# Kernel tuning notes

Hardware: AMD Instinct MI355X
Metric: run time of the kernel (lower is better)

Reference implementation:

```python
import jax, jax.numpy as jnp
import numpy as np

K = 7          # kernel_size
D = 1          # dilation
P = (D * (K - 1) + 1) // 2  # reflect padding = 3
N = 2
C_IN = 256
REL = 16
OUT = 256
SHARE = 8
H = 56
W = 56


def _unfold(x, k=K, d=D, p=P):
    # x: [n, c, h, w] -> [n, c, k*k, h*w], reflection-padded local windows
    n, c, h, w = x.shape
    xp = jnp.pad(x, ((0, 0), (0, 0), (p, p), (p, p)), mode='reflect')
    cols = [xp[:, :, i * d:i * d + h, j * d:j * d + w]
            for i in range(k) for j in range(k)]
    return jnp.stack(cols, axis=2).reshape(n, c, k * k, h * w)


def _conv1x1(x, w, b=None):
    # 1x1 conv == channel contraction; x: [n, c, *spatial]
    y = jnp.einsum('oc,nc...->no...', w, x)
    if b is not None:
        y = y + b.reshape((1, -1) + (1,) * (y.ndim - 2))
    return y


def _bn(x, g, b, eps=1e-5):
    # training-mode batchnorm over (N, *spatial) per channel; x: [n, c, a, b]
    m = x.mean(axis=(0, 2, 3), keepdims=True)
    v = x.var(axis=(0, 2, 3), keepdims=True)
    xh = (x - m) * jax.lax.rsqrt(v + eps)
    return xh * g.reshape(1, -1, 1, 1) + b.reshape(1, -1, 1, 1)


def _position(h, w):
    lw = jnp.broadcast_to(jnp.linspace(-1.0, 1.0, w)[None, :], (h, w))
    lh = jnp.broadcast_to(jnp.linspace(-1.0, 1.0, h)[:, None], (h, w))
    return jnp.stack([lw, lh], 0)[None]  # [1, 2, h, w]


def setup_inputs() -> dict:
    key = jax.random.key(0)
    ks = jax.random.split(key, 16)
    def rn(k, shape, s=0.05):
        return jax.random.normal(k, shape, jnp.float32) * s
    return dict(
        x=jax.random.normal(ks[0], (N, C_IN, H, W), jnp.float32),
        w1=rn(ks[1], (REL, C_IN)), b1=rn(ks[2], (REL,)),
        w2=rn(ks[3], (REL, C_IN)), b2=rn(ks[4], (REL,)),
        w3=rn(ks[5], (OUT, C_IN)), b3=rn(ks[6], (OUT,)),
        wp=rn(ks[7], (2, 2)), bp=rn(ks[8], (2,)),
        g1=jnp.ones(REL + 2, jnp.float32), be1=jnp.zeros(REL + 2, jnp.float32),
        cw1=rn(ks[9], (REL, REL + 2)),
        g2=jnp.ones(REL, jnp.float32), be2=jnp.zeros(REL, jnp.float32),
        cw2=rn(ks[10], (OUT // SHARE, REL)), cb2=rn(ks[11], (OUT // SHARE,)),
    )


def reference(x, w1, b1, w2, b2, w3, b3, wp, bp,
              g1, be1, cw1, g2, be2, cw2, cb2):
    n, _, h, w = x.shape
    hw = h * w
    x1 = _conv1x1(x, w1, b1)   # [n, rel, h, w]
    x2 = _conv1x1(x, w2, b2)   # [n, rel, h, w]
    x3 = _conv1x1(x, w3, b3)   # [n, out, h, w]
    pos = _conv1x1(_position(h, w), wp, bp)  # [1, 2, h, w]
    # Subtraction2: center query minus unfolded keys -> [n, rel, k^2, hw]
    sub2 = x1.reshape(n, REL, 1, hw) - _unfold(x2)
    # Subtraction on position: center minus neighbors -> [1, 2, k^2, hw]
    subp = pos.reshape(1, 2, 1, hw) - _unfold(pos)
    subp = jnp.broadcast_to(subp, (n, 2, K * K, hw))
    t = jnp.concatenate([sub2, subp], axis=1)           # [n, rel+2, k^2, hw]
    t = jax.nn.relu(_bn(t, g1, be1))
    t = _conv1x1(t, cw1)                                # [n, rel, k^2, hw]
    t = jax.nn.relu(_bn(t, g2, be2))
    wlog = _conv1x1(t, cw2, cb2)                        # [n, out//share, k^2, hw]
    ww = jax.nn.softmax(wlog, axis=-2)                  # softmax over k^2
    # Aggregation: gather values over windows and weight per share-group
    u3 = _unfold(x3).reshape(n, OUT // SHARE, SHARE, K * K, hw)
    out = jnp.einsum('ngskq,ngkq->ngsq', u3, ww).reshape(n, OUT, h, w)
    return out
```

## Files before the change

kernel.cpp:

```cpp
#include <hip/hip_runtime.h>
#include <hip/hip_bf16.h>
#include <cstdint>

#define HWS 3136
#define WID 56
#define NKQ 307328.0f
#define X3SCALE 2048.0f
#define X3INV   (1.0f / 2048.0f)
#define WQ      65535.0f

#define S_CW1 0
#define S_CW2 288
#define S_CB2 800
#define S_WP  832
#define S_G1  836
#define S_BE1 854
#define S_G2  872
#define S_BE2 888
#define S_TOT 904
#define NWT   73728

__device__ __forceinline__ int refl(int i) {
  if (i < 0) i = -i;
  if (i >= WID) i = 2 * WID - 2 - i;
  return i;
}

__global__ __launch_bounds__(256) void k_prep(
    const float* __restrict__ w1, const float* __restrict__ w2,
    const float* __restrict__ w3,
    const float* __restrict__ cw1, const float* __restrict__ cw2,
    const float* __restrict__ cb2, const float* __restrict__ wp,
    const float* __restrict__ g1, const float* __restrict__ be1,
    const float* __restrict__ g2, const float* __restrict__ be2,
    float* __restrict__ small, float* __restrict__ wT)
{
  int e = blockIdx.x * 256 + threadIdx.x;
  if (e < S_TOT) {
    float v;
    if (e < S_CW2)      v = cw1[e];
    else if (e < S_CB2) v = cw2[e - S_CW2];
    else if (e < S_WP)  v = cb2[e - S_CB2];
    else if (e < S_G1)  v = wp [e - S_WP];
    else if (e < S_BE1) v = g1 [e - S_G1];
    else if (e < S_G2)  v = be1[e - S_BE1];
    else if (e < S_BE2) v = g2 [e - S_G2];
    else                v = be2[e - S_BE2];
    small[e] = v;
  }
  int et = e - S_TOT;
  if (et >= 0 && et < NWT) {
    int c = et / 288, r = et - (et / 288) * 288;
    float v = (r < 16) ? w1[r * 256 + c]
            : (r < 32) ? w2[(r - 16) * 256 + c]
                       : w3[(r - 32) * 256 + c];
    wT[et] = v;
  }
}

__global__ __launch_bounds__(64) void k_proj(
    const float* __restrict__ x, const float* __restrict__ wT,
    const float* __restrict__ b1, const float* __restrict__ b2,
    const float* __restrict__ b3,
    float* __restrict__ x1t, float* __restrict__ x2t, short* __restrict__ x3i)
{
  const int lane = threadIdx.x;
  const int r0  = (blockIdx.x & 15) * 18;
  const int pck = blockIdx.x >> 4;
  const int P = pck * 64 + lane;
  const int n = P / HWS;

  float acc[18];
  #pragma unroll
  for (int i = 0; i < 18; i++) {
    int r = r0 + i;
    acc[i] = (r < 16) ? b1[r] : (r < 32) ? b2[r - 16] : b3[r - 32];
  }

  const float* xc = x + (size_t)n * 256 * HWS + (P - n * HWS);
  const float* wt0 = wT + r0;
  #pragma unroll 8
  for (int c = 0; c < 256; c++) {
    float xv = xc[(size_t)c * HWS];
    const float* wt = wt0 + c * 288;
    #pragma unroll
    for (int i = 0; i < 18; i++)
      acc[i] = fmaf(wt[i], xv, acc[i]);
  }

  #pragma unroll
  for (int i = 0; i < 18; i++) {
    int r = r0 + i;
    if (r < 16)
      x1t[(size_t)P * 16 + r] = acc[i];
    else if (r < 32)
      x2t[(size_t)P * 16 + (r - 16)] = acc[i];
    else {
      float cl = fminf(fmaxf(acc[i], -15.9f), 15.9f);
      x3i[(size_t)P * 256 + (r - 32)] = (short)__float2int_rn(cl * X3SCALE);
    }
  }
}

__global__ __launch_bounds__(256) void k_stats1(
    const float* __restrict__ x1t, const float* __restrict__ x2t,
    const float* __restrict__ small, float* __restrict__ gsum1)
{
  __shared__ float red[4][36];
  const int tid = threadIdx.x;
  const int bid = blockIdx.x;
  const int n = bid / 196;
  const int r = bid % 196;
  const int k = r >> 2, quar = r & 3;
  const int ki = k / 7 - 3, kj = k % 7 - 3;
  const float wp00 = small[S_WP+0], wp01 = small[S_WP+1];
  const float wp10 = small[S_WP+2], wp11 = small[S_WP+3];
  float s[18], ss[18];
  #pragma unroll
  for (int i = 0; i < 18; i++) { s[i] = 0.f; ss[i] = 0.f; }

  for (int qq = tid; qq < 784; qq += 256) {
    int q = quar * 784 + qq;
    int y = q / WID, xx = q - y * WID;
    int ny = refl(y + ki), nx = refl(xx + kj);
    int nb = ny * WID + nx;
    const float4* a = (const float4*)(x1t + (size_t)(n * HWS + q) * 16);
    const float4* b = (const float4*)(x2t + (size_t)(n * HWS + nb) * 16);
    #pragma unroll
    for (int r4 = 0; r4 < 4; r4++) {
      float4 av = a[r4], bv = b[r4];
      float v;
      v = av.x - bv.x; s[r4*4+0] += v; ss[r4*4+0] += v * v;
      v = av.y - bv.y; s[r4*4+1] += v; ss[r4*4+1] += v * v;
      v = av.z - bv.z; s[r4*4+2] += v; ss[r4*4+2] += v * v;
      v = av.w - bv.w; s[r4*4+3] += v; ss[r4*4+3] += v * v;
    }
    float dlw = (float)(xx - nx) * (2.f / 55.f);
    float dlh = (float)(y - ny) * (2.f / 55.f);
    float v16 = wp00 * dlw + wp01 * dlh;
    float v17 = wp10 * dlw + wp11 * dlh;
    s[16] += v16; ss[16] += v16 * v16;
    s[17] += v17; ss[17] += v17 * v17;
  }

  #pragma unroll
  for (int i = 0; i < 18; i++) {
    #pragma unroll
    for (int off = 32; off > 0; off >>= 1) {
      s[i]  += __shfl_down(s[i], off);
      ss[i] += __shfl_down(ss[i], off);
    }
  }
  const int wvv = tid >> 6, lane = tid & 63;
  if (lane == 0) {
    #pragma unroll
    for (int i = 0; i < 18; i++) { red[wvv][i] = s[i]; red[wvv][18 + i] = ss[i]; }
  }
  __syncthreads();
  if (tid < 36) {
    float t = red[0][tid] + red[1][tid] + red[2][tid] + red[3][tid];
    atomicAdd(&gsum1[tid], t);
  }
}

__global__ __launch_bounds__(256) void k_stats2(
    const float* __restrict__ x1t, const float* __restrict__ x2t,
    const float* __restrict__ small,
    const float* __restrict__ gsum1, float* __restrict__ gsum2)
{
  __shared__ float red[4][32];
  const int tid = threadIdx.x;
  const float inv = 1.f / NKQ;
  float sc1r[18], sh1r[18];
  #pragma unroll
  for (int c = 0; c < 18; c++) {
    float m = gsum1[c] * inv;
    float var = gsum1[18 + c] * inv - m * m;
    float sc = small[S_G1 + c] * rsqrtf(var + 1e-5f);
    sc1r[c] = sc; sh1r[c] = small[S_BE1 + c] - m * sc;
  }

  const int bid = blockIdx.x;
  const int n = bid / 196;
  const int r = bid % 196;
  const int k = r >> 2, quar = r & 3;
  const int ki = k / 7 - 3, kj = k % 7 - 3;
  const float wp00 = small[S_WP+0], wp01 = small[S_WP+1];
  const float wp10 = small[S_WP+2], wp11 = small[S_WP+3];
  const float* cw1f = small + S_CW1;
  float s[16], ss[16];
  #pragma unroll
  for (int i = 0; i < 16; i++) { s[i] = 0.f; ss[i] = 0.f; }

  for (int qq = tid; qq < 784; qq += 256) {
    int q = quar * 784 + qq;
    int y = q / WID, xx = q - y * WID;
    int ny = refl(y + ki), nx = refl(xx + kj);
    int nb = ny * WID + nx;
    float t1v[18];
    const float4* a4 = (const float4*)(x1t + (size_t)(n * HWS + q) * 16);
    const float4* b4 = (const float4*)(x2t + (size_t)(n * HWS + nb) * 16);
    #pragma unroll
    for (int r4 = 0; r4 < 4; r4++) {
      float4 av = a4[r4], bv = b4[r4];
      t1v[r4*4+0] = av.x - bv.x; t1v[r4*4+1] = av.y - bv.y;
      t1v[r4*4+2] = av.z - bv.z; t1v[r4*4+3] = av.w - bv.w;
    }
    float dlw = (float)(xx - nx) * (2.f / 55.f);
    float dlh = (float)(y - ny) * (2.f / 55.f);
    t1v[16] = wp00 * dlw + wp01 * dlh;
    t1v[17] = wp10 * dlw + wp11 * dlh;
    #pragma unroll
    for (int c = 0; c < 18; c++) t1v[c] = fmaxf(fmaf(t1v[c], sc1r[c], sh1r[c]), 0.f);
    #pragma unroll
    for (int r2 = 0; r2 < 16; r2++) {
      float acc = 0.f;
      #pragma unroll
      for (int c = 0; c < 18; c++) acc = fmaf(cw1f[r2 * 18 + c], t1v[c], acc);
      s[r2] += acc; ss[r2] += acc * acc;
    }
  }

  #pragma unroll
  for (int i = 0; i < 16; i++) {
    #pragma unroll
    for (int off = 32; off > 0; off >>= 1) {
      s[i]  += __shfl_down(s[i], off);
      ss[i] += __shfl_down(ss[i], off);
    }
  }
  const int wvv = tid >> 6, lane = tid & 63;
  if (lane == 0) {
    #pragma unroll
    for (int i = 0; i < 16; i++) { red[wvv][i] = s[i]; red[wvv][16 + i] = ss[i]; }
  }
  __syncthreads();
  if (tid < 32) {
    float t = red[0][tid] + red[1][tid] + red[2][tid] + red[3][tid];
    atomicAdd(&gsum2[tid], t);
  }
}

__global__ __launch_bounds__(256) void k_final(
    const float* __restrict__ x1t, const float* __restrict__ x2t,
    const short* __restrict__ x3i, const float* __restrict__ small,
    const float* __restrict__ gsum1, const float* __restrict__ gsum2,
    float* __restrict__ outf)
{
  __shared__ unsigned short wws[4][49][34];
  __shared__ int nbs[4][49];
  __shared__ float sc1s[18], sh1s[18], sc2s[16], sh2s[16];

  const int tid = threadIdx.x;
  const int lane = tid & 63;
  const int wv = tid >> 6;
  const float inv = 1.f / NKQ;

  if (tid < 18) {
    float m = gsum1[tid] * inv;
    float var = gsum1[18 + tid] * inv - m * m;
    float sc = small[S_G1 + tid] * rsqrtf(var + 1e-5f);
    sc1s[tid] = sc; sh1s[tid] = small[S_BE1 + tid] - m * sc;
  } else if (tid >= 32 && tid < 48) {
    int c = tid - 32;
    float m = gsum2[c] * inv;
    float var = gsum2[16 + c] * inv - m * m;
    float sc = small[S_G2 + c] * rsqrtf(var + 1e-5f);
    sc2s[c] = sc; sh2s[c] = small[S_BE2 + c] - m * sc;
  }
  __syncthreads();

  const int P = blockIdx.x * 4 + wv;
  const int n = P / HWS, q = P % HWS;
  const int y = q / WID, xx = q - y * WID;

  const bool valid = lane < 49;
  const int kk = valid ? lane : 48;
  const int ki = kk / 7 - 3, kj = kk % 7 - 3;
  const int ny = refl(y + ki), nx = refl(xx + kj);
  const int nb = ny * WID + nx;
  if (valid) nbs[wv][lane] = nb;

  float t1v[18];
  {
    const float4* a4 = (const float4*)(x1t + (size_t)(n * HWS + q) * 16);
    const float4* b4 = (const float4*)(x2t + (size_t)(n * HWS + nb) * 16);
    #pragma unroll
    for (int r4 = 0; r4 < 4; r4++) {
      float4 av = a4[r4], bv = b4[r4];
      t1v[r4*4+0] = av.x - bv.x; t1v[r4*4+1] = av.y - bv.y;
      t1v[r4*4+2] = av.z - bv.z; t1v[r4*4+3] = av.w - bv.w;
    }
    float dlw = (float)(xx - nx) * (2.f / 55.f);
    float dlh = (float)(y - ny) * (2.f / 55.f);
    t1v[16] = small[S_WP+0] * dlw + small[S_WP+1] * dlh;
    t1v[17] = small[S_WP+2] * dlw + small[S_WP+3] * dlh;
  }
  #pragma unroll
  for (int c = 0; c < 18; c++)
    t1v[c] = fmaxf(fmaf(t1v[c], sc1s[c], sh1s[c]), 0.f);

  float t2v[16];
  #pragma unroll
  for (int r = 0; r < 16; r++) {
    float acc = 0.f;
    #pragma unroll
    for (int c = 0; c < 18; c++) acc = fmaf(small[S_CW1 + r * 18 + c], t1v[c], acc);
    t2v[r] = fmaxf(fmaf(acc, sc2s[r], sh2s[r]), 0.f);
  }

  #pragma unroll
  for (int g = 0; g < 32; g++) {
    float acc = small[S_CB2 + g];
    #pragma unroll
    for (int r = 0; r < 16; r++) acc = fmaf(small[S_CW2 + g * 16 + r], t2v[r], acc);
    float e = valid ? __expf(acc) : 0.f;
    float s = e;
    #pragma unroll
    for (int off = 32; off >= 1; off >>= 1) s += __shfl_xor(s, off);
    if (valid)
      wws[wv][lane][g] = (unsigned short)__float2uint_rn(e / s * WQ);
  }
  __syncthreads();

  const short* x3p = x3i + (size_t)n * HWS * 256;
  const int* nbp = nbs[wv];
  const unsigned short (*wq)[34] = wws[wv];
  const int g0 = lane >> 3;
  float acc4[4] = {0.f, 0.f, 0.f, 0.f};
  #pragma unroll 7
  for (int k = 0; k < 49; k++) {
    const short* row = x3p + (size_t)nbp[k] * 256;
    #pragma unroll
    for (int ch = 0; ch < 4; ch++) {
      float w = (float)wq[k][ch * 8 + g0];
      acc4[ch] = fmaf(w, (float)row[ch * 64 + lane], acc4[ch]);
    }
  }
  const float osc = X3INV / WQ;
  #pragma unroll
  for (int ch = 0; ch < 4; ch++) {
    int o = ch * 64 + lane;
    outf[(size_t)(n * 256 + o) * HWS + q] = acc4[ch] * osc;
  }
}

extern "C" void kernel_launch(void* const* d_in, const int* in_sizes, int n_in,
                              void* d_out, int out_size, void* d_ws, size_t ws_size,
                              hipStream_t stream) {
  (void)in_sizes; (void)n_in; (void)out_size; (void)ws_size;
  char* ws = (char*)d_ws;
  float* gsum1 = (float*)(ws + 0);
  float* gsum2 = (float*)(ws + 160);
  float* small = (float*)(ws + 512);
  float* x1t   = (float*)(ws + 4608);
  float* x2t   = (float*)(ws + 406016);
  short* x3i   = (short*)(ws + 807424);
  float* outf  = (float*)d_out;
  float* wT    = (float*)d_out;

  const float* x   = (const float*)d_in[0];
  const float* w1  = (const float*)d_in[1];
  const float* b1  = (const float*)d_in[2];
  const float* w2  = (const float*)d_in[3];
  const float* b2  = (const float*)d_in[4];
  const float* w3  = (const float*)d_in[5];
  const float* b3  = (const float*)d_in[6];
  const float* wp  = (const float*)d_in[7];
  const float* g1  = (const float*)d_in[9];
  const float* be1 = (const float*)d_in[10];
  const float* cw1 = (const float*)d_in[11];
  const float* g2  = (const float*)d_in[12];
  const float* be2 = (const float*)d_in[13];
  const float* cw2 = (const float*)d_in[14];
  const float* cb2 = (const float*)d_in[15];

  hipMemsetAsync(d_ws, 0, 512, stream);
  k_prep<<<292, 256, 0, stream>>>(w1, w2, w3, cw1, cw2, cb2, wp,
                                  g1, be1, g2, be2, small, wT);
  k_proj<<<1568, 64, 0, stream>>>(x, wT, b1, b2, b3, x1t, x2t, x3i);
  k_stats1<<<392, 256, 0, stream>>>(x1t, x2t, small, gsum1);
  k_stats2<<<392, 256, 0, stream>>>(x1t, x2t, small, gsum1, gsum2);
  k_final<<<1568, 256, 0, stream>>>(x1t, x2t, x3i, small, gsum1, gsum2, outf);
}
```

Measured before the change: 200.9 us.

## Compute BN1 stats via box-filter algebra, defer softmax normalization, vectorize aggregation

Replaces the 49-offset brute-force pass for the first batchnorm statistics with an algebraic expansion. Sums of (x1 - x2_nb) and its square are rebuilt from x1 sums, x1 times a 7x7 reflect box sum of x2 (separable row and column passes), and x2 weighted by reflect multiplicity counts. The final kernel stores unnormalized exp weights in fp16 and divides by their accumulated sum at the end, which removes the per-group wave shuffle reduction. Each lane now loads four contiguous channels through an int2 read. stats2 gets twice as many blocks, and scratch space in the output buffer holds the box sums. The costs are extra launches and the fp32 cancellation risk in the 49*sum minus cross-term formula.

```diff
diff --git a/kernel.cpp b/kernel.cpp
--- a/kernel.cpp
+++ b/kernel.cpp
@@ -1,5 +1,6 @@
 #include <hip/hip_runtime.h>
 #include <hip/hip_bf16.h>
+#include <hip/hip_fp16.h>
 #include <cstdint>
 
 #define HWS 3136
@@ -7,7 +8,6 @@
 #define NKQ 307328.0f
 #define X3SCALE 2048.0f
 #define X3INV   (1.0f / 2048.0f)
-#define WQ      65535.0f
 
 #define S_CW1 0
 #define S_CW2 288
@@ -102,64 +102,131 @@
   }
 }
 
-__global__ __launch_bounds__(256) void k_stats1(
+__global__ __launch_bounds__(256) void k_rowbox(
+    const float* __restrict__ x2t, float* __restrict__ R)
+{
+  int idx = blockIdx.x * 256 + threadIdx.x;
+  int p = idx >> 2, cq = (idx & 3) * 4;
+  int n = p / HWS, q = p % HWS;
+  int y = q / WID, xx = q - y * WID;
+  float4 s = {0.f, 0.f, 0.f, 0.f};
+  #pragma unroll
+  for (int d = -3; d <= 3; d++) {
+    int nx = refl(xx + d);
+    float4 v = *(const float4*)(x2t + (size_t)(n * HWS + y * WID + nx) * 16 + cq);
+    s.x += v.x; s.y += v.y; s.z += v.z; s.w += v.w;
+  }
+  *(float4*)(R + (size_t)p * 16 + cq) = s;
+}
+
+__global__ __launch_bounds__(256) void k_bn1(
     const float* __restrict__ x1t, const float* __restrict__ x2t,
-    const float* __restrict__ small, float* __restrict__ gsum1)
-{
-  __shared__ float red[4][36];
+    const float* __restrict__ R, const float* __restrict__ small,
+    float* __restrict__ parts)
+{
+  __shared__ float cxs[56];
+  __shared__ float red[4][4][20];
+  __shared__ float pred[4][4];
   const int tid = threadIdx.x;
-  const int bid = blockIdx.x;
-  const int n = bid / 196;
-  const int r = bid % 196;
-  const int k = r >> 2, quar = r & 3;
-  const int ki = k / 7 - 3, kj = k % 7 - 3;
+  if (tid < 56) {
+    int cnt = 0;
+    for (int xx = 0; xx < 56; xx++)
+      for (int d = -3; d <= 3; d++)
+        if (refl(xx + d) == tid) cnt++;
+    cxs[tid] = (float)cnt;
+  }
+  __syncthreads();
+
+  const int idx = blockIdx.x * 256 + tid;
+  const int p = idx >> 2, cq = (idx & 3) * 4;
+  const int n = p / HWS, q = p % HWS;
+  const int y = q / WID, xx = q - y * WID;
+
+  float4 x1v = *(const float4*)(x1t + (size_t)p * 16 + cq);
+  float4 x2v = *(const float4*)(x2t + (size_t)p * 16 + cq);
+  float4 b2 = {0.f, 0.f, 0.f, 0.f};
+  #pragma unroll
+  for (int d = -3; d <= 3; d++) {
+    int ny = refl(y + d);
+    float4 v = *(const float4*)(R + (size_t)(n * HWS + ny * WID + xx) * 16 + cq);
+    b2.x += v.x; b2.y += v.y; b2.z += v.z; b2.w += v.w;
+  }
+  float cnt = cxs[y] * cxs[xx];
+
+  float a[20];
+  {
+    float xv[4] = {x1v.x, x1v.y, x1v.z, x1v.w};
+    float x2a[4] = {x2v.x, x2v.y, x2v.z, x2v.w};
+    float bb[4] = {b2.x, b2.y, b2.z, b2.w};
+    #pragma unroll
+    for (int j = 0; j < 4; j++) {
+      a[j*5+0] = xv[j];
+      a[j*5+1] = xv[j] * xv[j];
+      a[j*5+2] = xv[j] * bb[j];
+      a[j*5+3] = cnt * x2a[j];
+      a[j*5+4] = cnt * x2a[j] * x2a[j];
+    }
+  }
+  #pragma unroll
+  for (int i = 0; i < 20; i++) {
+    #pragma unroll
+    for (int off = 4; off <= 32; off <<= 1)
+      a[i] += __shfl_xor(a[i], off);
+  }
+  const int lane = tid & 63, wv = tid >> 6;
+  if (lane < 4) {
+    #pragma unroll
+    for (int i = 0; i < 20; i++) red[wv][lane][i] = a[i];
+  }
+
+  float ps[4] = {0.f, 0.f, 0.f, 0.f};
   const float wp00 = small[S_WP+0], wp01 = small[S_WP+1];
   const float wp10 = small[S_WP+2], wp11 = small[S_WP+3];
-  float s[18], ss[18];
-  #pragma unroll
-  for (int i = 0; i < 18; i++) { s[i] = 0.f; ss[i] = 0.f; }
-
-  for (int qq = tid; qq < 784; qq += 256) {
-    int q = quar * 784 + qq;
-    int y = q / WID, xx = q - y * WID;
-    int ny = refl(y + ki), nx = refl(xx + kj);
-    int nb = ny * WID + nx;
-    const float4* a = (const float4*)(x1t + (size_t)(n * HWS + q) * 16);
-    const float4* b = (const float4*)(x2t + (size_t)(n * HWS + nb) * 16);
-    #pragma unroll
-    for (int r4 = 0; r4 < 4; r4++) {
-      float4 av = a[r4], bv = b[r4];
-      float v;
-      v = av.x - bv.x; s[r4*4+0] += v; ss[r4*4+0] += v * v;
-      v = av.y - bv.y; s[r4*4+1] += v; ss[r4*4+1] += v * v;
-      v = av.z - bv.z; s[r4*4+2] += v; ss[r4*4+2] += v * v;
-      v = av.w - bv.w; s[r4*4+3] += v; ss[r4*4+3] += v * v;
-    }
-    float dlw = (float)(xx - nx) * (2.f / 55.f);
-    float dlh = (float)(y - ny) * (2.f / 55.f);
+  for (int it = idx; it < 153664; it += 25088) {
+    int k = it / 3136, qq = it - (it / 3136) * 3136;
+    int yy = qq / WID, xq = qq - yy * WID;
+    int ny = refl(yy + k / 7 - 3), nx = refl(xq + k % 7 - 3);
+    float dlw = (float)(xq - nx) * (2.f / 55.f);
+    float dlh = (float)(yy - ny) * (2.f / 55.f);
     float v16 = wp00 * dlw + wp01 * dlh;
     float v17 = wp10 * dlw + wp11 * dlh;
-    s[16] += v16; ss[16] += v16 * v16;
-    s[17] += v17; ss[17] += v17 * v17;
-  }
-
-  #pragma unroll
-  for (int i = 0; i < 18; i++) {
-    #pragma unroll
-    for (int off = 32; off > 0; off >>= 1) {
-      s[i]  += __shfl_down(s[i], off);
-      ss[i] += __shfl_down(ss[i], off);
-    }
-  }
-  const int wvv = tid >> 6, lane = tid & 63;
+    ps[0] += v16; ps[1] += v16 * v16;
+    ps[2] += v17; ps[3] += v17 * v17;
+  }
+  #pragma unroll
+  for (int i = 0; i < 4; i++) {
+    #pragma unroll
+    for (int off = 1; off <= 32; off <<= 1)
+      ps[i] += __shfl_xor(ps[i], off);
+  }
   if (lane == 0) {
     #pragma unroll
-    for (int i = 0; i < 18; i++) { red[wvv][i] = s[i]; red[wvv][18 + i] = ss[i]; }
+    for (int i = 0; i < 4; i++) pred[wv][i] = ps[i];
   }
   __syncthreads();
-  if (tid < 36) {
-    float t = red[0][tid] + red[1][tid] + red[2][tid] + red[3][tid];
-    atomicAdd(&gsum1[tid], t);
+
+  if (tid < 80) {
+    int cq2 = tid / 20, v = tid % 20;
+    float t = red[0][cq2][v] + red[1][cq2][v] + red[2][cq2][v] + red[3][cq2][v];
+    int c = cq2 * 4 + v / 5, qty = v % 5;
+    atomicAdd(&parts[c * 5 + qty], t);
+  } else if (tid < 84) {
+    int i = tid - 80;
+    float t = pred[0][i] + pred[1][i] + pred[2][i] + pred[3][i];
+    atomicAdd(&parts[80 + i], 2.0f * t);
+  }
+}
+
+__global__ void k_comb(const float* __restrict__ parts, float* __restrict__ gsum1)
+{
+  int tid = threadIdx.x;
+  if (tid < 16) {
+    const float* P = parts + tid * 5;
+    gsum1[tid]      = 49.f * P[0] - P[3];
+    gsum1[18 + tid] = 49.f * P[1] - 2.f * P[2] + P[4];
+  } else if (tid == 16) {
+    gsum1[16] = parts[80]; gsum1[17] = parts[82];
+    gsum1[34] = parts[81]; gsum1[35] = parts[83];
   }
 }
 
@@ -181,9 +248,9 @@
   }
 
   const int bid = blockIdx.x;
-  const int n = bid / 196;
-  const int r = bid % 196;
-  const int k = r >> 2, quar = r & 3;
+  const int n = bid / 392;
+  const int r = bid % 392;
+  const int k = r >> 3, eig = r & 7;
   const int ki = k / 7 - 3, kj = k % 7 - 3;
   const float wp00 = small[S_WP+0], wp01 = small[S_WP+1];
   const float wp10 = small[S_WP+2], wp11 = small[S_WP+3];
@@ -192,8 +259,8 @@
   #pragma unroll
   for (int i = 0; i < 16; i++) { s[i] = 0.f; ss[i] = 0.f; }
 
-  for (int qq = tid; qq < 784; qq += 256) {
-    int q = quar * 784 + qq;
+  for (int qq = tid; qq < 392; qq += 256) {
+    int q = eig * 392 + qq;
     int y = q / WID, xx = q - y * WID;
     int ny = refl(y + ki), nx = refl(xx + kj);
     int nb = ny * WID + nx;
@@ -247,7 +314,7 @@
     const float* __restrict__ gsum1, const float* __restrict__ gsum2,
     float* __restrict__ outf)
 {
-  __shared__ unsigned short wws[4][49][34];
+  __shared__ __half wwh[4][49][34];
   __shared__ int nbs[4][49];
   __shared__ float sc1s[18], sh1s[18], sc2s[16], sh2s[16];
 
@@ -310,39 +377,36 @@
   }
 
   #pragma unroll
-  for (int g = 0; g < 32; g++) {
-    float acc = small[S_CB2 + g];
-    #pragma unroll
-    for (int r = 0; r < 16; r++) acc = fmaf(small[S_CW2 + g * 16 + r], t2v[r], acc);
-    float e = valid ? __expf(acc) : 0.f;
-    float s = e;
-    #pragma unroll
-    for (int off = 32; off >= 1; off >>= 1) s += __shfl_xor(s, off);
-    if (valid)
-      wws[wv][lane][g] = (unsigned short)__float2uint_rn(e / s * WQ);
+  for (int g2 = 0; g2 < 32; g2++) {
+    float acc = small[S_CB2 + g2];
+    #pragma unroll
+    for (int r = 0; r < 16; r++) acc = fmaf(small[S_CW2 + g2 * 16 + r], t2v[r], acc);
+    if (valid) wwh[wv][lane][g2] = __float2half(__expf(acc));
   }
   __syncthreads();
 
   const short* x3p = x3i + (size_t)n * HWS * 256;
   const int* nbp = nbs[wv];
-  const unsigned short (*wq)[34] = wws[wv];
-  const int g0 = lane >> 3;
-  float acc4[4] = {0.f, 0.f, 0.f, 0.f};
+  const __half (*wh)[34] = wwh[wv];
+  const int g = lane >> 1;
+  const int o0 = lane * 4;
+  float acc0 = 0.f, acc1 = 0.f, acc2 = 0.f, acc3 = 0.f, wsum = 0.f;
   #pragma unroll 7
   for (int k = 0; k < 49; k++) {
-    const short* row = x3p + (size_t)nbp[k] * 256;
-    #pragma unroll
-    for (int ch = 0; ch < 4; ch++) {
-      float w = (float)wq[k][ch * 8 + g0];
-      acc4[ch] = fmaf(w, (float)row[ch * 64 + lane], acc4[ch]);
-    }
-  }
-  const float osc = X3INV / WQ;
-  #pragma unroll
-  for (int ch = 0; ch < 4; ch++) {
-    int o = ch * 64 + lane;
-    outf[(size_t)(n * 256 + o) * HWS + q] = acc4[ch] * osc;
-  }
+    const int2 d = *(const int2*)(x3p + (size_t)nbp[k] * 256 + o0);
+    float w = __half2float(wh[k][g]);
+    wsum += w;
+    acc0 = fmaf(w, (float)(short)(d.x & 0xffff), acc0);
+    acc1 = fmaf(w, (float)(short)(d.x >> 16),    acc1);
+    acc2 = fmaf(w, (float)(short)(d.y & 0xffff), acc2);
+    acc3 = fmaf(w, (float)(short)(d.y >> 16),    acc3);
+  }
+  const float sc = X3INV / wsum;
+  const size_t ob = (size_t)(n * 256 + o0) * HWS + q;
+  outf[ob]           = acc0 * sc;
+  outf[ob + HWS]     = acc1 * sc;
+  outf[ob + 2 * HWS] = acc2 * sc;
+  outf[ob + 3 * HWS] = acc3 * sc;
 }
 
 extern "C" void kernel_launch(void* const* d_in, const int* in_sizes, int n_in,
@@ -352,12 +416,14 @@
   char* ws = (char*)d_ws;
   float* gsum1 = (float*)(ws + 0);
   float* gsum2 = (float*)(ws + 160);
-  float* small = (float*)(ws + 512);
+  float* parts = (float*)(ws + 320);
+  float* small = (float*)(ws + 704);
   float* x1t   = (float*)(ws + 4608);
   float* x2t   = (float*)(ws + 406016);
   short* x3i   = (short*)(ws + 807424);
   float* outf  = (float*)d_out;
   float* wT    = (float*)d_out;
+  float* Rbox  = (float*)d_out + 262144;
 
   const float* x   = (const float*)d_in[0];
   const float* w1  = (const float*)d_in[1];
@@ -375,11 +441,13 @@
   const float* cw2 = (const float*)d_in[14];
   const float* cb2 = (const float*)d_in[15];
 
-  hipMemsetAsync(d_ws, 0, 512, stream);
+  hipMemsetAsync(d_ws, 0, 704, stream);
   k_prep<<<292, 256, 0, stream>>>(w1, w2, w3, cw1, cw2, cb2, wp,
                                   g1, be1, g2, be2, small, wT);
   k_proj<<<1568, 64, 0, stream>>>(x, wT, b1, b2, b3, x1t, x2t, x3i);
-  k_stats1<<<392, 256, 0, stream>>>(x1t, x2t, small, gsum1);
-  k_stats2<<<392, 256, 0, stream>>>(x1t, x2t, small, gsum1, gsum2);
+  k_rowbox<<<98, 256, 0, stream>>>(x2t, Rbox);
+  k_bn1<<<98, 256, 0, stream>>>(x1t, x2t, Rbox, small, parts);
+  k_comb<<<1, 64, 0, stream>>>(parts, gsum1);
+  k_stats2<<<784, 256, 0, stream>>>(x1t, x2t, small, gsum1, gsum2);
   k_final<<<1568, 256, 0, stream>>>(x1t, x2t, x3i, small, gsum1, gsum2, outf);
 }
```

After: 197.9 us. Within noise of the previous version (-1.5%).
